# Performance work log

Hardware: AMD Instinct MI355X
Metric: run time of the kernel (lower is better)

## Reference

```python
import jax, jax.numpy as jnp
import numpy as np

BRANCH, VOCAB, FFN, BATCH = 8, 256, 1024, 16384
LN_EPS = 1e-5


def setup_inputs() -> dict:
    key = jax.random.key(0)
    ks = jax.random.split(key, 7)
    x = jax.random.normal(ks[0], (BATCH, BRANCH, VOCAB), dtype=jnp.float32)
    U1 = 0.01 * jax.random.normal(ks[1], (BRANCH, VOCAB, FFN), dtype=jnp.float32)
    b1 = 0.01 * jax.random.normal(ks[2], (BRANCH, FFN), dtype=jnp.float32)
    U2 = 0.01 * jax.random.normal(ks[3], (BRANCH, FFN, VOCAB), dtype=jnp.float32)
    b2 = 0.01 * jax.random.normal(ks[4], (BRANCH, VOCAB), dtype=jnp.float32)
    ln_w = jnp.ones((VOCAB,), dtype=jnp.float32)
    ln_b = jnp.zeros((VOCAB,), dtype=jnp.float32)
    return {"x": x, "U1": U1, "b1": b1, "U2": U2, "b2": b2, "ln_w": ln_w, "ln_b": ln_b}


def _layernorm(h, w, b):
    mu = jnp.mean(h, axis=-1, keepdims=True)
    var = jnp.var(h, axis=-1, keepdims=True)
    return (h - mu) * jax.lax.rsqrt(var + LN_EPS) * w + b


def reference(x, U1, b1, U2, b2, ln_w, ln_b):
    # x: (B, N, D); branch-wise batched GEMMs via einsum (avoids explicit permutes)
    skip = x
    h = jnp.einsum('bnd,nde->bne', x, U1) + b1        # (B, N, FFN)
    h = jax.nn.gelu(h, approximate=False)
    h = jnp.einsum('bne,ned->bnd', h, U2) + b2        # (B, N, VOCAB)
    h = _layernorm(h, ln_w, ln_b)
    h = jax.nn.gelu(h, approximate=False)
    out = skip + h
    return out.reshape(BATCH, 1, BRANCH * VOCAB)
```

## Files before the change

kernel.cpp:

```cpp
#include <hip/hip_runtime.h>
#include <hip/hip_bf16.h>

#define NBR   8
#define DV    256
#define FF    1024
#define RT    64
#define NCH   32
#define NROWS 16384

#define L_B1 0
#define L_HS 32768
#define LDS_BYTES 36864

using bf16x8 = __attribute__((ext_vector_type(8))) short;
using f32x4  = __attribute__((ext_vector_type(4))) float;
using u32x4  = __attribute__((ext_vector_type(4))) unsigned int;

__device__ __forceinline__ unsigned short f2bf(float f) {
    unsigned int u = __builtin_bit_cast(unsigned int, f);
    unsigned int r = (u + 0x7fffu + ((u >> 16) & 1u)) >> 16;
    return (unsigned short)r;
}
__device__ __forceinline__ unsigned int f2bf_rhu(float f) {
    return (__builtin_bit_cast(unsigned int, f) + 0x8000u) >> 16;
}
__device__ __forceinline__ unsigned int pk_bf2(float a, float b) {
    unsigned int ua = __builtin_bit_cast(unsigned int, a) + 0x8000u;
    unsigned int ub = __builtin_bit_cast(unsigned int, b) + 0x8000u;
    return __builtin_amdgcn_perm(ub, ua, 0x07060302u);
}
__device__ __forceinline__ float gelu_fast(float x) {
    float x2 = x * x;
    float z  = x * fmaf(x2, -0.1029434959f, -2.3022078770f);
    float e  = __builtin_amdgcn_exp2f(z);
    return x * __builtin_amdgcn_rcpf(1.0f + e);
}

#define GLL(gsrc, ldst) __builtin_amdgcn_global_load_lds((const unsigned int*)(gsrc), (unsigned int*)(ldst), 16, 0, 0)
#define MFMA16 __builtin_amdgcn_mfma_f32_16x16x32_bf16

__global__ void prep_weights(const float* __restrict__ U1, const float* __restrict__ U2,
                             unsigned short* __restrict__ w1img, unsigned short* __restrict__ w2img)
{
    const int b = blockIdx.x;
    const int n = b >> 5, cch = b & 31;
    const int tid = threadIdx.x;
    char* img1 = (char*)w1img + ((size_t)b << 14);
    char* img2 = (char*)w2img + ((size_t)b << 14);
    const float* U1n = U1 + (size_t)n * DV * FF;
    const float* U2n = U2 + (size_t)n * FF * DV;
    #pragma unroll
    for (int e = 0; e < 4; ++e) {
        int p = tid + e * 256;
        int kkg = p >> 5, nn = p & 31;
        bf16x8 h;
        #pragma unroll
        for (int j = 0; j < 8; ++j)
            h[j] = (short)f2bf(U1n[(size_t)(kkg * 8 + j) * FF + cch * 32 + nn]);
        *(bf16x8*)(img1 + kkg * 512 + nn * 16) = h;
    }
    #pragma unroll
    for (int e = 0; e < 4; ++e) {
        int p = tid + e * 256;
        int cfg = p >> 6, l = p & 63;
        bf16x8 h;
        #pragma unroll
        for (int j = 0; j < 8; ++j)
            h[j] = (short)f2bf(U2n[(size_t)(cch * 32 + (l >> 4) * 8 + j) * DV + cfg * 16 + (l & 15)]);
        *(bf16x8*)(img2 + (p << 4)) = h;
    }
}

__global__ __launch_bounds__(512, 4)
void belayer_main(const float* __restrict__ x,
                  const unsigned short* __restrict__ w1img,
                  const unsigned short* __restrict__ w2img,
                  const float* __restrict__ b1g, const float* __restrict__ b2g,
                  const float* __restrict__ lnw, const float* __restrict__ lnb,
                  float* __restrict__ out)
{
    __shared__ __align__(16) char LDS[LDS_BYTES];
    const int tid  = threadIdx.x;
    const int lane = tid & 63;
    const int wave = tid >> 6;
    const int q = lane >> 4, c = lane & 15;
    const int n    = blockIdx.x & 7;
    const int tile = blockIdx.x >> 3;
    const int row0 = tile * RT;
    const int rowg   = wave >> 1;
    const int colsel = wave & 1;
    const int rowg2  = wave >> 2;
    const int colg2  = wave & 3;

    const char* g1base = (const char*)w1img + ((size_t)(n * NCH) << 14) + (wave << 11) + lane * 16;
    const char* g2img  = (const char*)w2img + ((size_t)(n * NCH) << 14) + (colg2 << 12) + lane * 16;
    char* l1base = LDS + L_B1 + (wave << 11);

#define STAGE1(T) do { const char* g_ = g1base + ((size_t)(T) << 14); \
        char* l_ = l1base + (((T) & 1) << 14); GLL(g_, l_); GLL(g_ + 1024, l_ + 1024); } while (0)

    STAGE1(0);

    bf16x8 A[8];
    {
        const float* src = x + (((size_t)(row0 + rowg * 16 + c)) * NBR + n) * DV + q * 8;
        #pragma unroll
        for (int ks = 0; ks < 8; ++ks) {
            f32x4 v0 = *(const f32x4*)(src + ks * 32);
            f32x4 v1 = *(const f32x4*)(src + ks * 32 + 4);
            u32x4 d;
            d[0] = pk_bf2(v0[0], v0[1]);
            d[1] = pk_bf2(v0[2], v0[3]);
            d[2] = pk_bf2(v1[0], v1[1]);
            d[3] = pk_bf2(v1[2], v1[3]);
            A[ks] = __builtin_bit_cast(bf16x8, d);
        }
    }

    const unsigned aB1 = (unsigned)(q * 512 + (colsel * 16 + c) * 16);
    unsigned aW[4];
    #pragma unroll
    for (int r = 0; r < 4; ++r)
        aW[r] = (unsigned)(((colsel * 2 + (c >> 3)) * 64 + rowg * 16 + q * 4 + r) * 16 + (c & 7) * 2);
    const unsigned aH = (unsigned)((q * 64 + rowg2 * 32 + c) * 16);

    float b2v[4];
    #pragma unroll
    for (int cf = 0; cf < 4; ++cf) b2v[cf] = b2g[n * DV + colg2 * 64 + cf * 16 + c];
    f32x4 acc2[2][4];
    #pragma unroll
    for (int i = 0; i < 2; ++i)
        #pragma unroll
        for (int j = 0; j < 4; ++j)
            acc2[i][j] = (f32x4){b2v[j], b2v[j], b2v[j], b2v[j]};

    __syncthreads();

    for (int t = 0; t < NCH; ++t) {
        const unsigned h1 = L_B1 + ((unsigned)(t & 1) << 14);

        bf16x8 B2f[4];
        #pragma unroll
        for (int cf = 0; cf < 4; ++cf)
            B2f[cf] = *(const bf16x8*)(g2img + ((size_t)t << 14) + (cf << 10));
        if (t + 1 < NCH) STAGE1(t + 1);
        float b1v = b1g[n * FF + t * 32 + colsel * 16 + c];
        f32x4 acc1 = (f32x4){b1v, b1v, b1v, b1v};
        #pragma unroll
        for (int ks = 0; ks < 8; ++ks) {
            bf16x8 b = *(const bf16x8*)(LDS + h1 + aB1 + ks * 2048);
            acc1 = MFMA16(A[ks], b, acc1, 0, 0, 0);
        }
        #pragma unroll
        for (int r = 0; r < 4; ++r) {
            float g = gelu_fast(acc1[r]);
            *(unsigned short*)(LDS + L_HS + aW[r]) = (unsigned short)f2bf_rhu(g);
        }
        __syncthreads();

        bf16x8 a0 = *(const bf16x8*)(LDS + L_HS + aH);
        bf16x8 a1 = *(const bf16x8*)(LDS + L_HS + aH + 256);
        #pragma unroll
        for (int cf = 0; cf < 4; ++cf) {
            acc2[0][cf] = MFMA16(a0, B2f[cf], acc2[0][cf], 0, 0, 0);
            acc2[1][cf] = MFMA16(a1, B2f[cf], acc2[1][cf], 0, 0, 0);
        }
        __syncthreads();
    }

    float sA[2][4], sQ[2][4];
    #pragma unroll
    for (int rf = 0; rf < 2; ++rf)
        #pragma unroll
        for (int r = 0; r < 4; ++r) { sA[rf][r] = 0.f; sQ[rf][r] = 0.f; }
    #pragma unroll
    for (int rf = 0; rf < 2; ++rf)
        #pragma unroll
        for (int cf = 0; cf < 4; ++cf)
            #pragma unroll
            for (int r = 0; r < 4; ++r) {
                float v = acc2[rf][cf][r];
                sA[rf][r] += v;
                sQ[rf][r] += v * v;
            }
    #pragma unroll
    for (int m = 1; m < 16; m <<= 1)
        #pragma unroll
        for (int rf = 0; rf < 2; ++rf)
            #pragma unroll
            for (int r = 0; r < 4; ++r) {
                sA[rf][r] += __shfl_xor(sA[rf][r], m, 64);
                sQ[rf][r] += __shfl_xor(sQ[rf][r], m, 64);
            }
    float* Lred = (float*)(LDS + L_HS);
    if (c == 0) {
        #pragma unroll
        for (int rf = 0; rf < 2; ++rf)
            #pragma unroll
            for (int r = 0; r < 4; ++r) {
                int row = rowg2 * 32 + rf * 16 + q * 4 + r;
                Lred[row * 4 + colg2]       = sA[rf][r];
                Lred[256 + row * 4 + colg2] = sQ[rf][r];
            }
    }
    __syncthreads();
    float mu[2][4], rs[2][4];
    #pragma unroll
    for (int rf = 0; rf < 2; ++rf)
        #pragma unroll
        for (int r = 0; r < 4; ++r) {
            int row = rowg2 * 32 + rf * 16 + q * 4 + r;
            f32x4 sv = *(const f32x4*)(Lred + row * 4);
            f32x4 qv = *(const f32x4*)(Lred + 256 + row * 4);
            float ssum = sv[0] + sv[1] + sv[2] + sv[3];
            float qsum = qv[0] + qv[1] + qv[2] + qv[3];
            float m_ = ssum * (1.0f / 256.0f);
            float var = qsum * (1.0f / 256.0f) - m_ * m_;
            mu[rf][r] = m_;
            rs[rf][r] = rsqrtf(var + 1e-5f);
        }
    #pragma unroll
    for (int cf = 0; cf < 4; ++cf) {
        int col = colg2 * 64 + cf * 16 + c;
        float lw = lnw[col];
        float lb = lnb[col];
        #pragma unroll
        for (int rf = 0; rf < 2; ++rf)
            #pragma unroll
            for (int r = 0; r < 4; ++r) {
                int row = rowg2 * 32 + rf * 16 + q * 4 + r;
                float v = (acc2[rf][cf][r] - mu[rf][r]) * rs[rf][r] * lw + lb;
                float g = gelu_fast(v);
                size_t oi = ((size_t)(row0 + row) * NBR + n) * DV + col;
                out[oi] = x[oi] + g;
            }
    }
#undef STAGE1
}

extern "C" void kernel_launch(void* const* d_in, const int* in_sizes, int n_in,
                              void* d_out, int out_size, void* d_ws, size_t ws_size,
                              hipStream_t stream) {
    const float* x   = (const float*)d_in[0];
    const float* U1  = (const float*)d_in[1];
    const float* b1  = (const float*)d_in[2];
    const float* U2  = (const float*)d_in[3];
    const float* b2  = (const float*)d_in[4];
    const float* lnw = (const float*)d_in[5];
    const float* lnb = (const float*)d_in[6];
    float* out = (float*)d_out;

    unsigned short* w1img = (unsigned short*)d_ws;
    unsigned short* w2img = w1img + (size_t)4 * 1024 * 1024 / 2;

    prep_weights<<<dim3(256), dim3(256), 0, stream>>>(U1, U2, w1img, w2img);
    belayer_main<<<dim3((NROWS / RT) * NBR), dim3(512), 0, stream>>>(x, w1img, w2img, b1, b2, lnw, lnb, out);
}
```

Before: 228.5 us.

## Double-buffer hidden tile, load W1 directly to registers, double row tile

Row tile grows from 64 to 128 with 1024-thread blocks. W1 fragments are now read straight from global memory into registers in MFMA-ready layout instead of being staged through LDS with global_load_lds. The GELU hidden tile is double-buffered, so the second GEMM for chunk t-1 runs in the same iteration as the first GEMM for chunk t, which cuts barriers to one per iteration. Block order is now branch-major, and the LDS footprint shrinks, at the cost of more register pressure and more global loads per wave.

```diff
diff --git a/kernel.cpp b/kernel.cpp
--- a/kernel.cpp
+++ b/kernel.cpp
@@ -4,13 +4,12 @@
 #define NBR   8
 #define DV    256
 #define FF    1024
-#define RT    64
+#define RT    128
 #define NCH   32
 #define NROWS 16384
 
-#define L_B1 0
-#define L_HS 32768
-#define LDS_BYTES 36864
+#define L_HS 0
+#define LDS_BYTES 16384
 
 using bf16x8 = __attribute__((ext_vector_type(8))) short;
 using f32x4  = __attribute__((ext_vector_type(4))) float;
@@ -36,7 +35,6 @@
     return x * __builtin_amdgcn_rcpf(1.0f + e);
 }
 
-#define GLL(gsrc, ldst) __builtin_amdgcn_global_load_lds((const unsigned int*)(gsrc), (unsigned int*)(ldst), 16, 0, 0)
 #define MFMA16 __builtin_amdgcn_mfma_f32_16x16x32_bf16
 
 __global__ void prep_weights(const float* __restrict__ U1, const float* __restrict__ U2,
@@ -52,12 +50,13 @@
     #pragma unroll
     for (int e = 0; e < 4; ++e) {
         int p = tid + e * 256;
-        int kkg = p >> 5, nn = p & 31;
+        int f = p >> 6, l = p & 63;
+        int ks = f >> 1, cf = f & 1;
         bf16x8 h;
         #pragma unroll
         for (int j = 0; j < 8; ++j)
-            h[j] = (short)f2bf(U1n[(size_t)(kkg * 8 + j) * FF + cch * 32 + nn]);
-        *(bf16x8*)(img1 + kkg * 512 + nn * 16) = h;
+            h[j] = (short)f2bf(U1n[(size_t)(ks * 32 + (l >> 4) * 8 + j) * FF + cch * 32 + cf * 16 + (l & 15)]);
+        *(bf16x8*)(img1 + (p << 4)) = h;
     }
     #pragma unroll
     for (int e = 0; e < 4; ++e) {
@@ -71,7 +70,7 @@
     }
 }
 
-__global__ __launch_bounds__(512, 4)
+__global__ __launch_bounds__(1024, 4)
 void belayer_main(const float* __restrict__ x,
                   const unsigned short* __restrict__ w1img,
                   const unsigned short* __restrict__ w2img,
@@ -84,22 +83,16 @@
     const int lane = tid & 63;
     const int wave = tid >> 6;
     const int q = lane >> 4, c = lane & 15;
-    const int n    = blockIdx.x & 7;
-    const int tile = blockIdx.x >> 3;
+    const int n    = blockIdx.x >> 7;
+    const int tile = blockIdx.x & 127;
     const int row0 = tile * RT;
     const int rowg   = wave >> 1;
     const int colsel = wave & 1;
     const int rowg2  = wave >> 2;
     const int colg2  = wave & 3;
 
-    const char* g1base = (const char*)w1img + ((size_t)(n * NCH) << 14) + (wave << 11) + lane * 16;
-    const char* g2img  = (const char*)w2img + ((size_t)(n * NCH) << 14) + (colg2 << 12) + lane * 16;
-    char* l1base = LDS + L_B1 + (wave << 11);
-
-#define STAGE1(T) do { const char* g_ = g1base + ((size_t)(T) << 14); \
-        char* l_ = l1base + (((T) & 1) << 14); GLL(g_, l_); GLL(g_ + 1024, l_ + 1024); } while (0)
-
-    STAGE1(0);
+    const char* g1img = (const char*)w1img + ((size_t)(n * NCH) << 14) + (colsel << 10) + lane * 16;
+    const char* g2img = (const char*)w2img + ((size_t)(n * NCH) << 14) + ((unsigned)(colg2 * 4) << 10) + lane * 16;
 
     bf16x8 A[8];
     {
@@ -117,12 +110,11 @@
         }
     }
 
-    const unsigned aB1 = (unsigned)(q * 512 + (colsel * 16 + c) * 16);
     unsigned aW[4];
     #pragma unroll
     for (int r = 0; r < 4; ++r)
-        aW[r] = (unsigned)(((colsel * 2 + (c >> 3)) * 64 + rowg * 16 + q * 4 + r) * 16 + (c & 7) * 2);
-    const unsigned aH = (unsigned)((q * 64 + rowg2 * 32 + c) * 16);
+        aW[r] = (unsigned)(((rowg * 16 + q * 4 + r) * 4 + (colsel * 2 + (c >> 3))) * 16 + (c & 7) * 2);
+    const unsigned aH = (unsigned)(((rowg2 * 32 + c) * 4 + q) * 16);
 
     float b2v[4];
     #pragma unroll
@@ -136,34 +128,44 @@
 
     __syncthreads();
 
-    for (int t = 0; t < NCH; ++t) {
-        const unsigned h1 = L_B1 + ((unsigned)(t & 1) << 14);
-
-        bf16x8 B2f[4];
-        #pragma unroll
-        for (int cf = 0; cf < 4; ++cf)
-            B2f[cf] = *(const bf16x8*)(g2img + ((size_t)t << 14) + (cf << 10));
-        if (t + 1 < NCH) STAGE1(t + 1);
-        float b1v = b1g[n * FF + t * 32 + colsel * 16 + c];
-        f32x4 acc1 = (f32x4){b1v, b1v, b1v, b1v};
-        #pragma unroll
-        for (int ks = 0; ks < 8; ++ks) {
-            bf16x8 b = *(const bf16x8*)(LDS + h1 + aB1 + ks * 2048);
-            acc1 = MFMA16(A[ks], b, acc1, 0, 0, 0);
-        }
-        #pragma unroll
-        for (int r = 0; r < 4; ++r) {
-            float g = gelu_fast(acc1[r]);
-            *(unsigned short*)(LDS + L_HS + aW[r]) = (unsigned short)f2bf_rhu(g);
-        }
-        __syncthreads();
-
-        bf16x8 a0 = *(const bf16x8*)(LDS + L_HS + aH);
-        bf16x8 a1 = *(const bf16x8*)(LDS + L_HS + aH + 256);
-        #pragma unroll
-        for (int cf = 0; cf < 4; ++cf) {
-            acc2[0][cf] = MFMA16(a0, B2f[cf], acc2[0][cf], 0, 0, 0);
-            acc2[1][cf] = MFMA16(a1, B2f[cf], acc2[1][cf], 0, 0, 0);
+    for (int t = 0; t <= NCH; ++t) {
+        if (t < NCH) {
+            const char* g1 = g1img + ((size_t)t << 14);
+            bf16x8 Ba[4], Bb[4];
+            #pragma unroll
+            for (int ks = 0; ks < 4; ++ks)
+                Ba[ks] = *(const bf16x8*)(g1 + (ks << 11));
+            float b1v = b1g[n * FF + t * 32 + colsel * 16 + c];
+            f32x4 acc1 = (f32x4){b1v, b1v, b1v, b1v};
+            #pragma unroll
+            for (int ks = 0; ks < 4; ++ks)
+                acc1 = MFMA16(A[ks], Ba[ks], acc1, 0, 0, 0);
+            #pragma unroll
+            for (int ks = 0; ks < 4; ++ks)
+                Bb[ks] = *(const bf16x8*)(g1 + ((ks + 4) << 11));
+            #pragma unroll
+            for (int ks = 0; ks < 4; ++ks)
+                acc1 = MFMA16(A[ks + 4], Bb[ks], acc1, 0, 0, 0);
+            const unsigned hw = L_HS + ((unsigned)(t & 1) << 13);
+            #pragma unroll
+            for (int r = 0; r < 4; ++r) {
+                float g = gelu_fast(acc1[r]);
+                *(unsigned short*)(LDS + hw + aW[r]) = (unsigned short)f2bf_rhu(g);
+            }
+        }
+        if (t >= 1) {
+            bf16x8 B2f[4];
+            #pragma unroll
+            for (int cf = 0; cf < 4; ++cf)
+                B2f[cf] = *(const bf16x8*)(g2img + ((size_t)(t - 1) << 14) + (cf << 10));
+            const unsigned hp = L_HS + ((unsigned)((t - 1) & 1) << 13);
+            bf16x8 a0 = *(const bf16x8*)(LDS + hp + aH);
+            bf16x8 a1 = *(const bf16x8*)(LDS + hp + aH + 1024);
+            #pragma unroll
+            for (int cf = 0; cf < 4; ++cf) {
+                acc2[0][cf] = MFMA16(a0, B2f[cf], acc2[0][cf], 0, 0, 0);
+                acc2[1][cf] = MFMA16(a1, B2f[cf], acc2[1][cf], 0, 0, 0);
+            }
         }
         __syncthreads();
     }
@@ -200,7 +202,7 @@
             for (int r = 0; r < 4; ++r) {
                 int row = rowg2 * 32 + rf * 16 + q * 4 + r;
                 Lred[row * 4 + colg2]       = sA[rf][r];
-                Lred[256 + row * 4 + colg2] = sQ[rf][r];
+                Lred[512 + row * 4 + colg2] = sQ[rf][r];
             }
     }
     __syncthreads();
@@ -211,7 +213,7 @@
         for (int r = 0; r < 4; ++r) {
             int row = rowg2 * 32 + rf * 16 + q * 4 + r;
             f32x4 sv = *(const f32x4*)(Lred + row * 4);
-            f32x4 qv = *(const f32x4*)(Lred + 256 + row * 4);
+            f32x4 qv = *(const f32x4*)(Lred + 512 + row * 4);
             float ssum = sv[0] + sv[1] + sv[2] + sv[3];
             float qsum = qv[0] + qv[1] + qv[2] + qv[3];
             float m_ = ssum * (1.0f / 256.0f);
@@ -235,7 +237,6 @@
                 out[oi] = x[oi] + g;
             }
     }
-#undef STAGE1
 }
 
 extern "C" void kernel_launch(void* const* d_in, const int* in_sizes, int n_in,
@@ -254,5 +255,5 @@
     unsigned short* w2img = w1img + (size_t)4 * 1024 * 1024 / 2;
 
     prep_weights<<<dim3(256), dim3(256), 0, stream>>>(U1, U2, w1img, w2img);
-    belayer_main<<<dim3((NROWS / RT) * NBR), dim3(512), 0, stream>>>(x, w1img, w2img, b1, b2, lnw, lnb, out);
-}
+    belayer_main<<<dim3(NBR * (NROWS / RT)), dim3(1024), 0, stream>>>(x, w1img, w2img, b1, b2, lnw, lnb, out);
+}
```

After: 323.5 us. 41.6% more time.
